# Kernel tuning notes

Measured on AMD Instinct MI355X. Metric: run time of the kernel, lower is better.

The kernel has to match this reference:

```python
import jax, jax.numpy as jnp
import numpy as np

DIM = 256
EXPAND = 2
INNER = DIM * EXPAND
EPS = 1e-6


def setup_inputs() -> dict:
    key = jax.random.key(0)
    ks = jax.random.split(key, 4)
    B, L = 8, 512
    x = jax.random.normal(ks[0], (B, L, DIM), dtype=jnp.float32)
    Win = jax.random.normal(ks[1], (2 * INNER, DIM), dtype=jnp.float32) * (DIM ** -0.5)
    conv_w = jax.random.normal(ks[2], (INNER, 1, 3), dtype=jnp.float32) * (3 ** -0.5)
    state_decay = jnp.zeros((INNER,), dtype=jnp.float32)
    state_scale = jnp.ones((INNER,), dtype=jnp.float32)
    Wout = jax.random.normal(ks[3], (DIM, INNER), dtype=jnp.float32) * (INNER ** -0.5)
    norm_w = jnp.ones((DIM,), dtype=jnp.float32)
    return {"x": x, "Win": Win, "conv_w": conv_w, "state_decay": state_decay,
            "state_scale": state_scale, "Wout": Wout, "norm_w": norm_w}


def _rmsnorm(y, w):
    ms = jnp.mean(jnp.square(y), axis=-1, keepdims=True)
    return y * jax.lax.rsqrt(ms + EPS) * w


def reference(x, Win, conv_w, state_decay, state_scale, Wout, norm_w):
    B, L, _ = x.shape
    # input projection, split into u (ssm path) and g (gate)
    xp = jnp.einsum('bld,ed->ble', x, Win)  # [B, L, 2*inner]
    u, g = jnp.split(xp, 2, axis=-1)
    # causal depthwise conv (left pad 2, kernel 3)
    u_t = jnp.pad(jnp.swapaxes(u, 1, 2), ((0, 0), (0, 0), (2, 0)))  # [B, inner, L+2]
    u_t = jax.lax.conv_general_dilated(
        u_t, conv_w, window_strides=(1,), padding=[(0, 0)],
        dimension_numbers=('NCH', 'OIH', 'NCH'), feature_group_count=INNER)
    u = jnp.swapaxes(u_t, 1, 2)  # [B, L, inner]
    d = jax.nn.sigmoid(state_decay)
    inp = (1.0 - d) * state_scale * u  # [B, L, inner]
    log_d = jnp.log(jnp.maximum(d, 1e-6))
    t_idx = jnp.arange(L, dtype=x.dtype)
    diff = t_idx[:, None] - t_idx[None, :]  # [L, L]
    causal = (diff >= 0).astype(x.dtype)
    # M[t, k, d] = d^(t-k) for k <= t, else 0  -> [L, L, inner]
    M = jnp.exp(jnp.maximum(diff, 0.0)[:, :, None] * log_d) * causal[:, :, None]
    y = jnp.einsum('tkd,bkd->btd', M, inp) * jax.nn.sigmoid(g)
    out = jnp.einsum('bti,oi->bto', y, Wout)  # [B, L, dim]
    return _rmsnorm(out, norm_w)
```

## Files before the change

### kernel.cpp

```cpp
#include <hip/hip_runtime.h>

#define B_     8
#define L_     512
#define DIM_   256
#define INNER_ 512
#define M_ROWS (B_*L_)

typedef __bf16 bf16x8 __attribute__((ext_vector_type(8)));
typedef float  fl4    __attribute__((ext_vector_type(4)));

typedef const __attribute__((address_space(1))) void gvoid;
typedef __attribute__((address_space(3))) void lvoid;

__device__ __forceinline__ void gl_lds16(const void* g, void* l) {
    __builtin_amdgcn_global_load_lds((gvoid*)g, (lvoid*)l, 16, 0, 0);
}
__device__ __forceinline__ unsigned short f2bf(float f) {
    unsigned int u = __float_as_uint(f);
    u = (u + 0x7fffu + ((u >> 16) & 1u)) >> 16;
    return (unsigned short)u;
}
__device__ __forceinline__ ushort4 f4bf4(float4 v) {
    union { __bf16 h[4]; ushort4 u; } r;
    r.h[0] = (__bf16)v.x; r.h[1] = (__bf16)v.y;
    r.h[2] = (__bf16)v.z; r.h[3] = (__bf16)v.w;
    return r.u;
}

__global__ __launch_bounds__(256) void conv_wout(const float* __restrict__ wout,
                                                 unsigned short* __restrict__ woutb)
{
    const int i4 = blockIdx.x * blockDim.x + threadIdx.x;
    float4 v = *(const float4*)&wout[(size_t)i4*4];
    *(ushort4*)&woutb[(size_t)i4*4] = f4bf4(v);
}

__global__ __launch_bounds__(512) void p1_fused(
    const float* __restrict__ x, const float* __restrict__ Win,
    const float* __restrict__ convw, const float* __restrict__ sdecay,
    const float* __restrict__ sscale,
    unsigned short* __restrict__ yb)
{
    constexpr int BK = 64;
    constexpr int LDA = BK + 8;
    __shared__ __align__(16) char smem[80*1024];
    unsigned short* As = (unsigned short*)smem;
    unsigned short* Bs = (unsigned short*)(smem + 73728);
    float* u_lds = (float*)smem;
    float* g_lds = (float*)(smem + 34816);
    float* carry = (float*)(smem + 69632);

    const int tid  = threadIdx.x;
    const int wave = tid >> 6, lane = tid & 63;
    const int b  = blockIdx.x >> 5;
    const int cg = blockIdx.x & 31;

    fl4 acc[4][2] = {};

    const int kc = (tid & 15) * 4;
    const int rsub = tid >> 4;

    for (int kt = 0; kt < DIM_; kt += BK) {
        __syncthreads();
        #pragma unroll
        for (int p = 0; p < 16; ++p) {
            const int l = p*32 + rsub;
            float4 v = *(const float4*)&x[(size_t)(b*L_ + l)*DIM_ + kt + kc];
            *(ushort4*)&As[l*LDA + kc] = f4bf4(v);
        }
        {
            const int wrow = (rsub < 16) ? (cg*16 + rsub) : (INNER_ + cg*16 + (rsub-16));
            float4 v = *(const float4*)&Win[(size_t)wrow*DIM_ + kt + kc];
            *(ushort4*)&Bs[rsub*LDA + kc] = f4bf4(v);
        }
        __syncthreads();

        #pragma unroll
        for (int kh = 0; kh < 2; ++kh) {
            bf16x8 af[4], bfr[2];
            #pragma unroll
            for (int m = 0; m < 4; ++m)
                af[m] = *(const bf16x8*)&As[(wave*64 + m*16 + (lane & 15))*LDA + kh*32 + (lane >> 4)*8];
            #pragma unroll
            for (int n = 0; n < 2; ++n)
                bfr[n] = *(const bf16x8*)&Bs[(n*16 + (lane & 15))*LDA + kh*32 + (lane >> 4)*8];
            #pragma unroll
            for (int m = 0; m < 4; ++m)
                #pragma unroll
                for (int n = 0; n < 2; ++n)
                    acc[m][n] = __builtin_amdgcn_mfma_f32_16x16x32_bf16(af[m], bfr[n], acc[m][n], 0, 0, 0);
        }
    }

    __syncthreads();
    #pragma unroll
    for (int m = 0; m < 4; ++m)
        #pragma unroll
        for (int r = 0; r < 4; ++r) {
            const int l = wave*64 + m*16 + (lane >> 4)*4 + r;
            const int c2 = lane & 15;
            u_lds[l*17 + c2] = acc[m][0][r];
            g_lds[l*17 + c2] = acc[m][1][r];
        }
    __syncthreads();

    {
        const int c2 = tid & 15;
        const int j  = tid >> 4;
        const int c  = cg*16 + c2;

        const float draw = 1.0f / (1.0f + __expf(-sdecay[c]));
        const float deff = fmaxf(draw, 1e-6f);
        const float ins  = (1.0f - draw) * sscale[c];
        const float w0 = convw[c*3+0], w1 = convw[c*3+1], w2 = convw[c*3+2];

        const int l0 = j*16;
        float um1 = (l0 >= 1) ? u_lds[(l0-1)*17 + c2] : 0.f;
        float um2 = (l0 >= 2) ? u_lds[(l0-2)*17 + c2] : 0.f;

        float sloc[16];
        float s = 0.f;
        #pragma unroll
        for (int i = 0; i < 16; ++i) {
            const float u = u_lds[(l0+i)*17 + c2];
            const float uc = fmaf(w2, u, fmaf(w1, um1, w0*um2));
            um2 = um1; um1 = u;
            s = fmaf(deff, s, ins*uc);
            sloc[i] = s;
        }
        carry[j*16 + c2] = s;
        __syncthreads();
        const float dp16 = __powf(deff, 16.0f);
        float s0 = 0.f;
        for (int i = 0; i < j; ++i) s0 = fmaf(s0, dp16, carry[i*16 + c2]);

        float pw = 1.0f;
        #pragma unroll
        for (int i = 0; i < 16; ++i) {
            pw *= deff;
            const float sv   = fmaf(s0, pw, sloc[i]);
            const float gate = 1.0f / (1.0f + __expf(-g_lds[(l0+i)*17 + c2]));
            yb[(size_t)(b*L_ + l0 + i)*INNER_ + c] = f2bf(sv * gate);
        }
    }
}

__global__ __launch_bounds__(512) void p3_gemm2(
    const unsigned short* __restrict__ yb,
    const unsigned short* __restrict__ woutb,
    const float* __restrict__ normw,
    float* __restrict__ out)
{
    __shared__ __align__(16) char smem[36*1024];
    unsigned short* As2 = (unsigned short*)smem;
    unsigned short* Bs2 = (unsigned short*)(smem + 2048);
    float* ssp = (float*)(smem + 2048 + 32768);
    const int tid  = threadIdx.x;
    const int wave = tid >> 6, lane = tid & 63;
    const int row0 = blockIdx.x * 16;
    const int wc   = wave * 32;
    fl4 acc[2] = {};
    for (int kt = 0; kt < INNER_; kt += 64) {
        __syncthreads();
        for (int ch = wave; ch < 34; ch += 8) {
            const int ke = (lane & 7) * 8;
            if (ch < 2)
                gl_lds16(yb    + (size_t)(row0 + ch*8 + (lane >> 3))*INNER_ + kt + ke,
                         (char*)As2 + ch*1024);
            else
                gl_lds16(woutb + (size_t)((ch-2)*8 + (lane >> 3))*INNER_ + kt + ke,
                         (char*)Bs2 + (ch-2)*1024);
        }
        __syncthreads();
        #pragma unroll
        for (int kh = 0; kh < 2; ++kh) {
            bf16x8 a = *(const bf16x8*)&As2[(lane & 15)*64 + kh*32 + (lane >> 4)*8];
            #pragma unroll
            for (int n = 0; n < 2; ++n) {
                bf16x8 b = *(const bf16x8*)&Bs2[(wc + n*16 + (lane & 15))*64 + kh*32 + (lane >> 4)*8];
                acc[n] = __builtin_amdgcn_mfma_f32_16x16x32_bf16(a, b, acc[n], 0, 0, 0);
            }
        }
    }
    float t[4];
    #pragma unroll
    for (int q = 0; q < 4; ++q) {
        float s = 0.f;
        #pragma unroll
        for (int n = 0; n < 2; ++n) { const float v = acc[n][q]; s = fmaf(v, v, s); }
        s += __shfl_xor(s, 1, 64); s += __shfl_xor(s, 2, 64);
        s += __shfl_xor(s, 4, 64); s += __shfl_xor(s, 8, 64);
        t[q] = s;
    }
    if ((lane & 15) == 0) {
        #pragma unroll
        for (int q = 0; q < 4; ++q)
            ssp[((lane >> 4)*4 + q)*8 + wave] = t[q];
    }
    __syncthreads();
    #pragma unroll
    for (int q = 0; q < 4; ++q) {
        const int rl = (lane >> 4)*4 + q;
        float ss = 0.f;
        #pragma unroll
        for (int w = 0; w < 8; ++w) ss += ssp[rl*8 + w];
        const float rf = rsqrtf(ss * (1.0f/DIM_) + 1e-6f);
        #pragma unroll
        for (int n = 0; n < 2; ++n) {
            const int col = wc + n*16 + (lane & 15);
            out[(size_t)(row0 + rl)*DIM_ + col] = acc[n][q] * rf * normw[col];
        }
    }
}

extern "C" void kernel_launch(void* const* d_in, const int* in_sizes, int n_in,
                              void* d_out, int out_size, void* d_ws, size_t ws_size,
                              hipStream_t stream)
{
    const float* x      = (const float*)d_in[0];
    const float* Win    = (const float*)d_in[1];
    const float* convw  = (const float*)d_in[2];
    const float* sdecay = (const float*)d_in[3];
    const float* sscale = (const float*)d_in[4];
    const float* Wout   = (const float*)d_in[5];
    const float* normw  = (const float*)d_in[6];
    float* out = (float*)d_out;

    char* ws = (char*)d_ws;
    unsigned short* woutb = (unsigned short*)(ws);
    unsigned short* yb    = (unsigned short*)(ws + (1u<<20));

    conv_wout<<<128, 256, 0, stream>>>(Wout, woutb);
    p1_fused<<<256, 512, 0, stream>>>(x, Win, convw, sdecay, sscale, yb);
    p3_gemm2<<<256, 512, 0, stream>>>(yb, woutb, normw, out);
}
```

Baseline: 36.94 us.

## Pre-convert inputs to bf16 and feed MFMA directly from global memory

A single conversion kernel now turns x, Win and Wout to bf16 in workspace, replacing the Wout-only conversion. Both GEMM stages drop their LDS staging and barriers and load MFMA operands straight from global memory, relying on L2 for reuse. Block-to-work mapping is also reordered so that adjacent blocks share weight columns. In exchange, x makes an extra round trip through memory, and operand reuse that LDS used to capture now depends on cache hits.

```diff
diff --git a/kernel.cpp b/kernel.cpp
--- a/kernel.cpp
+++ b/kernel.cpp
@@ -9,12 +9,6 @@
 typedef __bf16 bf16x8 __attribute__((ext_vector_type(8)));
 typedef float  fl4    __attribute__((ext_vector_type(4)));
 
-typedef const __attribute__((address_space(1))) void gvoid;
-typedef __attribute__((address_space(3))) void lvoid;
-
-__device__ __forceinline__ void gl_lds16(const void* g, void* l) {
-    __builtin_amdgcn_global_load_lds((gvoid*)g, (lvoid*)l, 16, 0, 0);
-}
 __device__ __forceinline__ unsigned short f2bf(float f) {
     unsigned int u = __float_as_uint(f);
     u = (u + 0x7fffu + ((u >> 16) & 1u)) >> 16;
@@ -27,81 +21,68 @@
     return r.u;
 }
 
-__global__ __launch_bounds__(256) void conv_wout(const float* __restrict__ wout,
-                                                 unsigned short* __restrict__ woutb)
-{
-    const int i4 = blockIdx.x * blockDim.x + threadIdx.x;
-    float4 v = *(const float4*)&wout[(size_t)i4*4];
-    *(ushort4*)&woutb[(size_t)i4*4] = f4bf4(v);
+__global__ __launch_bounds__(256) void convert_all(
+    const float* __restrict__ x, const float* __restrict__ win,
+    const float* __restrict__ wout,
+    unsigned short* __restrict__ xb, unsigned short* __restrict__ winb,
+    unsigned short* __restrict__ woutb)
+{
+    const int NX4 = (M_ROWS*DIM_) / 4;
+    const int NW4 = (2*INNER_*DIM_) / 4;
+    const int NO4 = (DIM_*INNER_) / 4;
+    int i4 = blockIdx.x * blockDim.x + threadIdx.x;
+    const float* src; unsigned short* dst; int off;
+    if (i4 < NX4)             { src = x;    dst = xb;    off = i4; }
+    else if (i4 < NX4+NW4)    { src = win;  dst = winb;  off = i4 - NX4; }
+    else                      { src = wout; dst = woutb; off = i4 - NX4 - NW4; }
+    float4 v = *(const float4*)&src[(size_t)off*4];
+    *(ushort4*)&dst[(size_t)off*4] = f4bf4(v);
 }
 
 __global__ __launch_bounds__(512) void p1_fused(
-    const float* __restrict__ x, const float* __restrict__ Win,
+    const unsigned short* __restrict__ xb, const unsigned short* __restrict__ winb,
     const float* __restrict__ convw, const float* __restrict__ sdecay,
     const float* __restrict__ sscale,
     unsigned short* __restrict__ yb)
 {
-    constexpr int BK = 64;
-    constexpr int LDA = BK + 8;
-    __shared__ __align__(16) char smem[80*1024];
-    unsigned short* As = (unsigned short*)smem;
-    unsigned short* Bs = (unsigned short*)(smem + 73728);
+    __shared__ __align__(16) char smem[72*1024];
     float* u_lds = (float*)smem;
     float* g_lds = (float*)(smem + 34816);
     float* carry = (float*)(smem + 69632);
 
     const int tid  = threadIdx.x;
     const int wave = tid >> 6, lane = tid & 63;
-    const int b  = blockIdx.x >> 5;
-    const int cg = blockIdx.x & 31;
-
-    fl4 acc[4][2] = {};
-
-    const int kc = (tid & 15) * 4;
-    const int rsub = tid >> 4;
-
-    for (int kt = 0; kt < DIM_; kt += BK) {
-        __syncthreads();
-        #pragma unroll
-        for (int p = 0; p < 16; ++p) {
-            const int l = p*32 + rsub;
-            float4 v = *(const float4*)&x[(size_t)(b*L_ + l)*DIM_ + kt + kc];
-            *(ushort4*)&As[l*LDA + kc] = f4bf4(v);
-        }
-        {
-            const int wrow = (rsub < 16) ? (cg*16 + rsub) : (INNER_ + cg*16 + (rsub-16));
-            float4 v = *(const float4*)&Win[(size_t)wrow*DIM_ + kt + kc];
-            *(ushort4*)&Bs[rsub*LDA + kc] = f4bf4(v);
-        }
-        __syncthreads();
-
-        #pragma unroll
-        for (int kh = 0; kh < 2; ++kh) {
-            bf16x8 af[4], bfr[2];
+    const int b  = blockIdx.x & 7;
+    const int cg = blockIdx.x >> 3;
+    const int r15 = lane & 15, q = lane >> 4;
+
+    {
+        const size_t arow0 = ((size_t)(b*L_ + wave*64 + r15)) * DIM_;
+        const size_t urow  = ((size_t)(cg*16 + r15)) * DIM_;
+        const size_t grow  = ((size_t)(INNER_ + cg*16 + r15)) * DIM_;
+
+        fl4 acc[4][2] = {};
+        #pragma unroll
+        for (int kt = 0; kt < DIM_; kt += 32) {
+            const int ko = kt + q*8;
+            const bf16x8 bu = *(const bf16x8*)&winb[urow + ko];
+            const bf16x8 bg = *(const bf16x8*)&winb[grow + ko];
             #pragma unroll
-            for (int m = 0; m < 4; ++m)
-                af[m] = *(const bf16x8*)&As[(wave*64 + m*16 + (lane & 15))*LDA + kh*32 + (lane >> 4)*8];
+            for (int m = 0; m < 4; ++m) {
+                const bf16x8 a = *(const bf16x8*)&xb[arow0 + (size_t)m*16*DIM_ + ko];
+                acc[m][0] = __builtin_amdgcn_mfma_f32_16x16x32_bf16(a, bu, acc[m][0], 0, 0, 0);
+                acc[m][1] = __builtin_amdgcn_mfma_f32_16x16x32_bf16(a, bg, acc[m][1], 0, 0, 0);
+            }
+        }
+        #pragma unroll
+        for (int m = 0; m < 4; ++m)
             #pragma unroll
-            for (int n = 0; n < 2; ++n)
-                bfr[n] = *(const bf16x8*)&Bs[(n*16 + (lane & 15))*LDA + kh*32 + (lane >> 4)*8];
-            #pragma unroll
-            for (int m = 0; m < 4; ++m)
-                #pragma unroll
-                for (int n = 0; n < 2; ++n)
-                    acc[m][n] = __builtin_amdgcn_mfma_f32_16x16x32_bf16(af[m], bfr[n], acc[m][n], 0, 0, 0);
-        }
-    }
-
-    __syncthreads();
-    #pragma unroll
-    for (int m = 0; m < 4; ++m)
-        #pragma unroll
-        for (int r = 0; r < 4; ++r) {
-            const int l = wave*64 + m*16 + (lane >> 4)*4 + r;
-            const int c2 = lane & 15;
-            u_lds[l*17 + c2] = acc[m][0][r];
-            g_lds[l*17 + c2] = acc[m][1][r];
-        }
+            for (int r = 0; r < 4; ++r) {
+                const int l = wave*64 + m*16 + q*4 + r;
+                u_lds[l*17 + r15] = acc[m][0][r];
+                g_lds[l*17 + r15] = acc[m][1][r];
+            }
+    }
     __syncthreads();
 
     {
@@ -151,64 +132,56 @@
     const float* __restrict__ normw,
     float* __restrict__ out)
 {
-    __shared__ __align__(16) char smem[36*1024];
-    unsigned short* As2 = (unsigned short*)smem;
-    unsigned short* Bs2 = (unsigned short*)(smem + 2048);
-    float* ssp = (float*)(smem + 2048 + 32768);
+    __shared__ float ssp[16*8];
     const int tid  = threadIdx.x;
     const int wave = tid >> 6, lane = tid & 63;
-    const int row0 = blockIdx.x * 16;
+    const int r15 = lane & 15, q = lane >> 4;
+    const int row0 = (blockIdx.x & 7)*L_ + (blockIdx.x >> 3)*16;
     const int wc   = wave * 32;
+
     fl4 acc[2] = {};
-    for (int kt = 0; kt < INNER_; kt += 64) {
-        __syncthreads();
-        for (int ch = wave; ch < 34; ch += 8) {
-            const int ke = (lane & 7) * 8;
-            if (ch < 2)
-                gl_lds16(yb    + (size_t)(row0 + ch*8 + (lane >> 3))*INNER_ + kt + ke,
-                         (char*)As2 + ch*1024);
-            else
-                gl_lds16(woutb + (size_t)((ch-2)*8 + (lane >> 3))*INNER_ + kt + ke,
-                         (char*)Bs2 + (ch-2)*1024);
-        }
-        __syncthreads();
-        #pragma unroll
-        for (int kh = 0; kh < 2; ++kh) {
-            bf16x8 a = *(const bf16x8*)&As2[(lane & 15)*64 + kh*32 + (lane >> 4)*8];
-            #pragma unroll
-            for (int n = 0; n < 2; ++n) {
-                bf16x8 b = *(const bf16x8*)&Bs2[(wc + n*16 + (lane & 15))*64 + kh*32 + (lane >> 4)*8];
-                acc[n] = __builtin_amdgcn_mfma_f32_16x16x32_bf16(a, b, acc[n], 0, 0, 0);
-            }
-        }
-    }
+    {
+        const size_t abase = ((size_t)(row0 + r15)) * INNER_;
+        const size_t bb0   = ((size_t)(wc + r15)) * INNER_;
+        const size_t bb1   = ((size_t)(wc + 16 + r15)) * INNER_;
+        #pragma unroll
+        for (int kt = 0; kt < INNER_; kt += 32) {
+            const int ko = kt + q*8;
+            const bf16x8 a = *(const bf16x8*)&yb[abase + ko];
+            acc[0] = __builtin_amdgcn_mfma_f32_16x16x32_bf16(
+                         a, *(const bf16x8*)&woutb[bb0 + ko], acc[0], 0, 0, 0);
+            acc[1] = __builtin_amdgcn_mfma_f32_16x16x32_bf16(
+                         a, *(const bf16x8*)&woutb[bb1 + ko], acc[1], 0, 0, 0);
+        }
+    }
+
     float t[4];
     #pragma unroll
-    for (int q = 0; q < 4; ++q) {
+    for (int qq = 0; qq < 4; ++qq) {
         float s = 0.f;
         #pragma unroll
-        for (int n = 0; n < 2; ++n) { const float v = acc[n][q]; s = fmaf(v, v, s); }
+        for (int n = 0; n < 2; ++n) { const float v = acc[n][qq]; s = fmaf(v, v, s); }
         s += __shfl_xor(s, 1, 64); s += __shfl_xor(s, 2, 64);
         s += __shfl_xor(s, 4, 64); s += __shfl_xor(s, 8, 64);
-        t[q] = s;
-    }
-    if ((lane & 15) == 0) {
-        #pragma unroll
-        for (int q = 0; q < 4; ++q)
-            ssp[((lane >> 4)*4 + q)*8 + wave] = t[q];
+        t[qq] = s;
+    }
+    if (r15 == 0) {
+        #pragma unroll
+        for (int qq = 0; qq < 4; ++qq)
+            ssp[(q*4 + qq)*8 + wave] = t[qq];
     }
     __syncthreads();
     #pragma unroll
-    for (int q = 0; q < 4; ++q) {
-        const int rl = (lane >> 4)*4 + q;
+    for (int qq = 0; qq < 4; ++qq) {
+        const int rl = q*4 + qq;
         float ss = 0.f;
         #pragma unroll
         for (int w = 0; w < 8; ++w) ss += ssp[rl*8 + w];
         const float rf = rsqrtf(ss * (1.0f/DIM_) + 1e-6f);
         #pragma unroll
         for (int n = 0; n < 2; ++n) {
-            const int col = wc + n*16 + (lane & 15);
-            out[(size_t)(row0 + rl)*DIM_ + col] = acc[n][q] * rf * normw[col];
+            const int col = wc + n*16 + r15;
+            out[(size_t)(row0 + rl)*DIM_ + col] = acc[n][qq] * rf * normw[col];
         }
     }
 }
@@ -227,10 +200,12 @@
     float* out = (float*)d_out;
 
     char* ws = (char*)d_ws;
-    unsigned short* woutb = (unsigned short*)(ws);
-    unsigned short* yb    = (unsigned short*)(ws + (1u<<20));
-
-    conv_wout<<<128, 256, 0, stream>>>(Wout, woutb);
-    p1_fused<<<256, 512, 0, stream>>>(x, Win, convw, sdecay, sscale, yb);
+    unsigned short* xb    = (unsigned short*)(ws);
+    unsigned short* winb  = (unsigned short*)(ws + (2u<<20));
+    unsigned short* woutb = (unsigned short*)(ws + (2u<<20) + (512u<<10));
+    unsigned short* yb    = (unsigned short*)(ws + (3u<<20));
+
+    convert_all<<<1408, 256, 0, stream>>>(x, Win, Wout, xb, winb, woutb);
+    p1_fused<<<256, 512, 0, stream>>>(xb, winb, convw, sdecay, sscale, yb);
     p3_gemm2<<<256, 512, 0, stream>>>(yb, woutb, normw, out);
 }
```

After: 38.22 us. 1.03x slower.
